# Optimization experiments

Measured on AMD Instinct MI355X. Metric: run time of the kernel, lower is better.

The kernel has to match this reference:

```python
import jax, jax.numpy as jnp
import numpy as np

N, L, S, H, D = 2, 2048, 2048, 8, 64

def elu_feature_map(x):
    return jax.nn.elu(x) + 1.0

def setup_inputs() -> dict:
    key = jax.random.key(0)
    k1, k2, k3, k4, k5 = jax.random.split(key, 5)
    return {
        "queries": jax.random.normal(k1, (N, L, H, D), dtype=jnp.float32),
        "keys": jax.random.normal(k2, (N, S, H, D), dtype=jnp.float32),
        "values": jax.random.normal(k3, (N, S, H, D), dtype=jnp.float32),
        "q_mask": jnp.ones((N, L), dtype=jnp.float32),
        "kv_mask": jnp.ones((N, S), dtype=jnp.float32),
        "W": jax.random.normal(k4, (1, 2), dtype=jnp.float32) * 0.5,  # nn.Linear(2,1) weight
        "b": jax.random.normal(k5, (1,), dtype=jnp.float32) * 0.5,    # nn.Linear(2,1) bias
    }

def reference(queries, keys, values, q_mask, kv_mask, W, b):
    # feature map: elu(x) + 1
    Q = elu_feature_map(queries) * q_mask[:, :, None, None]   # [N,L,H,D]
    K = elu_feature_map(keys) * kv_mask[:, :, None, None]     # [N,S,H,D]
    queries_m = queries * q_mask[:, :, None, None]
    values_m = values * kv_mask[:, :, None, None]  # masked but unused downstream (as in original)
    del values_m
    # full QK score tensor [N,L,S,H]
    qk = jnp.einsum('nlhd,nshd->nlsh', Q, K)
    qk_mean = jnp.mean(qk, axis=2)  # [N,L,H]
    qk_max = jnp.max(qk, axis=2)    # [N,L,H]
    stats = jnp.stack([qk_mean, qk_max], axis=-1)  # [N,L,H,2]
    gate = jax.nn.sigmoid(jnp.einsum('nlhe,oe->nlho', stats, W) + b)  # [N,L,H,1]
    atten = gate[..., 0]  # [N,L,H]
    return queries_m * atten[..., None]  # [N,L,H,D]
```

## Files before the change

### kernel.cpp

```cpp
#include <hip/hip_runtime.h>
#include <math.h>

#define N_ 2
#define L_ 2048
#define S_ 2048
#define H_ 8
#define D_ 64

#define BLK_L 256
#define BS 64
#define SSPLIT 4

typedef __attribute__((ext_vector_type(8))) short short8;
typedef _Float16 half8 __attribute__((ext_vector_type(8)));
typedef __attribute__((ext_vector_type(16))) float floatx16;

__device__ __forceinline__ float feat(float x) {
    return x > 0.0f ? x + 1.0f : __expf(x);
}
__device__ __forceinline__ void gload_lds16(const void* g, void* l) {
    __builtin_amdgcn_global_load_lds(
        (__attribute__((address_space(1))) void*)g,
        (__attribute__((address_space(3))) void*)l, 16, 0, 0);
}

__global__ __launch_bounds__(256) void featk_kernel(
        const float* __restrict__ K, const float* __restrict__ kvmask,
        short* __restrict__ Khi, short* __restrict__ Klo,
        float* __restrict__ Ksum) {
    __shared__ float sm[64][68];
    __shared__ float sm2[256];
    int nh = blockIdx.x;
    int z  = blockIdx.y;
    int n = nh >> 3, h = nh & 7;
    int t = threadIdx.x;
    int srow = t >> 2, g = t & 3;
    int s = z * 64 + srow;

    float km = kvmask[n * S_ + s];
    const float* kp = K + (((size_t)n * S_ + s) * H_ + h) * D_ + g * 16;
    float fv[16];
    #pragma unroll
    for (int j = 0; j < 4; ++j) {
        float4 v = *(const float4*)(kp + j * 4);
        fv[4 * j + 0] = feat(v.x) * km;
        fv[4 * j + 1] = feat(v.y) * km;
        fv[4 * j + 2] = feat(v.z) * km;
        fv[4 * j + 3] = feat(v.w) * km;
    }
    half8 h0, h1, l0, l1;
    #pragma unroll
    for (int j = 0; j < 8; ++j) {
        _Float16 hb = (_Float16)fv[j];
        h0[j] = hb;  l0[j] = (_Float16)(fv[j] - (float)hb);
        _Float16 hb2 = (_Float16)fv[8 + j];
        h1[j] = hb2; l1[j] = (_Float16)(fv[8 + j] - (float)hb2);
    }
    size_t rowbase = ((size_t)nh * S_ + s) * (size_t)D_;
    int rx = srow & 7;
    *(half8*)(Khi + rowbase + ((((2 * g)    ) ^ rx) << 3)) = h0;
    *(half8*)(Khi + rowbase + ((((2 * g) + 1) ^ rx) << 3)) = h1;
    *(half8*)(Klo + rowbase + ((((2 * g)    ) ^ rx) << 3)) = l0;
    *(half8*)(Klo + rowbase + ((((2 * g) + 1) ^ rx) << 3)) = l1;

    #pragma unroll
    for (int j2 = 0; j2 < 4; ++j2)
        *(float4*)&sm[srow][g * 16 + 4 * j2] =
            make_float4(fv[4 * j2], fv[4 * j2 + 1], fv[4 * j2 + 2], fv[4 * j2 + 3]);
    __syncthreads();
    {
        int d = t & 63, grp = t >> 6;
        float part = 0.f;
        #pragma unroll
        for (int k = 0; k < 16; ++k) part += sm[grp * 16 + k][d];
        sm2[t] = part;
    }
    __syncthreads();
    if (t < 64) {
        float tot = sm2[t] + sm2[t + 64] + sm2[t + 128] + sm2[t + 192];
        atomicAdd(&Ksum[nh * 64 + t], tot);
    }
}

__global__ __launch_bounds__(256, 2) void rowmax_mfma(
        const float* __restrict__ Q, const short* __restrict__ Khi,
        const short* __restrict__ Klo, const float* __restrict__ qmask,
        float* __restrict__ rowmaxg) {
    __shared__ __align__(16) char lds[2][16384];

    int flat = blockIdx.x + (blockIdx.y << 3) + (blockIdx.z << 7);
    int nid  = ((flat & 7) << 6) | (flat >> 3);
    int bx = nid & 7;
    int nh = (nid >> 3) & 15;
    int z  = nid >> 7;

    int n = nh >> 3, h = nh & 7;
    int t = threadIdx.x;
    int w = t >> 6, lane = t & 63;
    int c31 = lane & 31, hi32 = lane >> 5;
    int lblock = bx * BLK_L;

    const char* gKh = (const char*)Khi + ((size_t)nh * S_ + (size_t)z * (S_ / SSPLIT)) * 128;
    const char* gKl = (const char*)Klo + ((size_t)nh * S_ + (size_t)z * (S_ / SSPLIT)) * 128;
    int sidx = w << 2;

    auto stage = [&](int tile, int db) {
        #pragma unroll
        for (int c = 0; c < 4; ++c) {
            int idx = sidx | c;
            const char* src = (idx < 8 ? gKh : gKl)
                              + tile * 8192 + ((idx & 7) << 10) + (lane << 4);
            gload_lds16(src, &lds[db][idx << 10]);
        }
    };

    stage(0, 0);

    half8 Ah[2][4], Al[2][4];
    #pragma unroll
    for (int lt = 0; lt < 2; ++lt) {
        int lrow = lblock + w * 64 + lt * 32 + c31;
        float qm = qmask[n * L_ + lrow];
        const float* qp = Q + (((size_t)n * L_ + lrow) * H_ + h) * D_ + hi32 * 8;
        #pragma unroll
        for (int ks = 0; ks < 4; ++ks) {
            float4 v0 = *(const float4*)(qp + ks * 16);
            float4 v1 = *(const float4*)(qp + ks * 16 + 4);
            float fv[8];
            fv[0] = feat(v0.x) * qm; fv[1] = feat(v0.y) * qm;
            fv[2] = feat(v0.z) * qm; fv[3] = feat(v0.w) * qm;
            fv[4] = feat(v1.x) * qm; fv[5] = feat(v1.y) * qm;
            fv[6] = feat(v1.z) * qm; fv[7] = feat(v1.w) * qm;
            half8 hi, lo;
            #pragma unroll
            for (int j = 0; j < 8; ++j) {
                _Float16 hb = (_Float16)fv[j];
                hi[j] = hb;
                lo[j] = (_Float16)(fv[j] - (float)hb);
            }
            Ah[lt][ks] = hi;
            Al[lt][ks] = lo;
        }
    }

    int boff[2][4];
    #pragma unroll
    for (int st = 0; st < 2; ++st)
        #pragma unroll
        for (int ks = 0; ks < 4; ++ks) {
            int row = st * 32 + c31;
            boff[st][ks] = row * 128 + (((2 * ks + hi32) ^ (row & 7)) << 4);
        }

    float rmax[2][16];
    #pragma unroll
    for (int i = 0; i < 2; ++i)
        #pragma unroll
        for (int r = 0; r < 16; ++r) rmax[i][r] = 0.f;

    const floatx16 Z = {0.f};

    __syncthreads();

    const int tiles = S_ / SSPLIT / BS;
    for (int tile = 0; tile < tiles; ++tile) {
        int db = tile & 1;
        if (tile + 1 < tiles) stage(tile + 1, db ^ 1);
        const char* hp = lds[db];
        const char* lp = lds[db] + 8192;
        #pragma unroll
        for (int st = 0; st < 2; ++st) {
            half8 Bh[4], Bl[4];
            #pragma unroll
            for (int ks = 0; ks < 4; ++ks) {
                Bh[ks] = *(const half8*)(hp + boff[st][ks]);
                Bl[ks] = *(const half8*)(lp + boff[st][ks]);
            }
            #pragma unroll
            for (int lt = 0; lt < 2; ++lt) {
                floatx16 acc;
                acc = __builtin_amdgcn_mfma_f32_32x32x16_f16(Ah[lt][0], Bh[0], Z,   0, 0, 0);
                acc = __builtin_amdgcn_mfma_f32_32x32x16_f16(Ah[lt][1], Bh[1], acc, 0, 0, 0);
                acc = __builtin_amdgcn_mfma_f32_32x32x16_f16(Ah[lt][2], Bh[2], acc, 0, 0, 0);
                acc = __builtin_amdgcn_mfma_f32_32x32x16_f16(Ah[lt][3], Bh[3], acc, 0, 0, 0);
                acc = __builtin_amdgcn_mfma_f32_32x32x16_f16(Ah[lt][0], Bl[0], acc, 0, 0, 0);
                acc = __builtin_amdgcn_mfma_f32_32x32x16_f16(Ah[lt][1], Bl[1], acc, 0, 0, 0);
                acc = __builtin_amdgcn_mfma_f32_32x32x16_f16(Ah[lt][2], Bl[2], acc, 0, 0, 0);
                acc = __builtin_amdgcn_mfma_f32_32x32x16_f16(Ah[lt][3], Bl[3], acc, 0, 0, 0);
                acc = __builtin_amdgcn_mfma_f32_32x32x16_f16(Al[lt][0], Bh[0], acc, 0, 0, 0);
                acc = __builtin_amdgcn_mfma_f32_32x32x16_f16(Al[lt][1], Bh[1], acc, 0, 0, 0);
                acc = __builtin_amdgcn_mfma_f32_32x32x16_f16(Al[lt][2], Bh[2], acc, 0, 0, 0);
                acc = __builtin_amdgcn_mfma_f32_32x32x16_f16(Al[lt][3], Bh[3], acc, 0, 0, 0);
                #pragma unroll
                for (int r = 0; r < 16; ++r)
                    rmax[lt][r] = fmaxf(rmax[lt][r], acc[r]);
            }
        }
        __syncthreads();
    }

    #pragma unroll
    for (int lt = 0; lt < 2; ++lt)
        #pragma unroll
        for (int r = 0; r < 16; ++r) {
            float m = rmax[lt][r];
            m = fmaxf(m, __shfl_xor(m, 1, 64));
            m = fmaxf(m, __shfl_xor(m, 2, 64));
            m = fmaxf(m, __shfl_xor(m, 4, 64));
            m = fmaxf(m, __shfl_xor(m, 8, 64));
            m = fmaxf(m, __shfl_xor(m, 16, 64));
            if (c31 == 0) {
                int l = lblock + w * 64 + lt * 32 + (r & 3) + ((r >> 2) << 3) + (hi32 << 2);
                atomicMax((unsigned*)&rowmaxg[(size_t)nh * L_ + l],
                          __float_as_uint(m));
            }
        }
}

__global__ __launch_bounds__(256) void finalize_kernel(
        const float* __restrict__ Q, const float* __restrict__ qmask,
        const float* __restrict__ Ksum, const float* __restrict__ rowmaxg,
        const float* __restrict__ W, const float* __restrict__ b,
        float* __restrict__ out) {
    int t = threadIdx.x;
    int lane = t & 63;
    int wid = (blockIdx.x << 2) | (t >> 6);
    int n = wid / (L_ * H_);
    int lh = wid % (L_ * H_);
    int l = lh / H_, h = lh % H_;

    float q = Q[(size_t)wid * 64 + lane];
    float qm = qmask[n * L_ + l];
    float p = feat(q) * qm * Ksum[(n * H_ + h) * 64 + lane];
    #pragma unroll
    for (int off = 32; off > 0; off >>= 1)
        p += __shfl_xor(p, off, 64);
    float mean = p * (1.0f / S_);
    float mx = rowmaxg[((size_t)n * H_ + h) * L_ + l];
    float zz = W[0] * mean + W[1] * mx + b[0];
    float g = 1.0f / (1.0f + __expf(-zz));
    out[(size_t)wid * 64 + lane] = q * qm * g;
}

extern "C" void kernel_launch(void* const* d_in, const int* in_sizes, int n_in,
                              void* d_out, int out_size, void* d_ws, size_t ws_size,
                              hipStream_t stream) {
    const float* Q      = (const float*)d_in[0];
    const float* K      = (const float*)d_in[1];
    const float* qmask  = (const float*)d_in[3];
    const float* kvmask = (const float*)d_in[4];
    const float* W      = (const float*)d_in[5];
    const float* b      = (const float*)d_in[6];
    float* out = (float*)d_out;

    float* Ksum   = (float*)d_ws;
    float* rowmax = (float*)d_ws + 1024;
    short* Khi    = (short*)((float*)d_ws + 1024 + 32768);
    short* Klo    = Khi + (size_t)N_ * H_ * S_ * D_;

    hipMemsetAsync(d_ws, 0, (1024 + (size_t)N_ * H_ * L_) * sizeof(float), stream);

    featk_kernel<<<dim3(N_ * H_, S_ / 64), 256, 0, stream>>>(K, kvmask, Khi, Klo, Ksum);
    rowmax_mfma<<<dim3(L_ / BLK_L, N_ * H_, SSPLIT), 256, 0, stream>>>(
        Q, Khi, Klo, qmask, rowmax);
    finalize_kernel<<<dim3(N_ * L_ * H_ / 4), 256, 0, stream>>>(
        Q, qmask, Ksum, rowmax, W, b, out);
}
```

Baseline: 118.5 us.

## Drop memset and atomics, use bf16 split MFMA, 512-thread blocks, vectorized finalize

Removes the workspace memset by writing per-block partial K sums and per-split row maxima instead of atomics, and reduces them later: Ksum inside the rowmax kernel, the four split maxima in finalize. Switches the hi/lo split product from fp16 to bf16 MFMA with manual round-to-nearest conversion. Doubles the rowmax block to 512 threads with one 32-row tile per wave, and vectorizes finalize to float4 per thread with 16-lane reductions. The bf16 hi/lo split keeps fewer mantissa bits than fp16 hi/lo, which risks accuracy. The Ksum reduction inside rowmax_mfma is not ordered before finalize within the same kernel, but finalize runs as a later launch, so it is safe.

```diff
diff --git a/kernel.cpp b/kernel.cpp
--- a/kernel.cpp
+++ b/kernel.cpp
@@ -12,11 +12,18 @@
 #define SSPLIT 4
 
 typedef __attribute__((ext_vector_type(8))) short short8;
-typedef _Float16 half8 __attribute__((ext_vector_type(8)));
 typedef __attribute__((ext_vector_type(16))) float floatx16;
 
 __device__ __forceinline__ float feat(float x) {
     return x > 0.0f ? x + 1.0f : __expf(x);
+}
+__device__ __forceinline__ short f2bf(float x) {
+    unsigned u = __float_as_uint(x);
+    unsigned r = (u + 0x7fffu + ((u >> 16) & 1u)) >> 16;
+    return (short)r;
+}
+__device__ __forceinline__ float bf2f(short h) {
+    return __uint_as_float(((unsigned)(unsigned short)h) << 16);
 }
 __device__ __forceinline__ void gload_lds16(const void* g, void* l) {
     __builtin_amdgcn_global_load_lds(
@@ -27,7 +34,7 @@
 __global__ __launch_bounds__(256) void featk_kernel(
         const float* __restrict__ K, const float* __restrict__ kvmask,
         short* __restrict__ Khi, short* __restrict__ Klo,
-        float* __restrict__ Ksum) {
+        float* __restrict__ Kpart) {
     __shared__ float sm[64][68];
     __shared__ float sm2[256];
     int nh = blockIdx.x;
@@ -48,20 +55,20 @@
         fv[4 * j + 2] = feat(v.z) * km;
         fv[4 * j + 3] = feat(v.w) * km;
     }
-    half8 h0, h1, l0, l1;
+    short8 h0, h1, l0, l1;
     #pragma unroll
     for (int j = 0; j < 8; ++j) {
-        _Float16 hb = (_Float16)fv[j];
-        h0[j] = hb;  l0[j] = (_Float16)(fv[j] - (float)hb);
-        _Float16 hb2 = (_Float16)fv[8 + j];
-        h1[j] = hb2; l1[j] = (_Float16)(fv[8 + j] - (float)hb2);
+        short hb = f2bf(fv[j]);
+        h0[j] = hb;  l0[j] = f2bf(fv[j] - bf2f(hb));
+        short hb2 = f2bf(fv[8 + j]);
+        h1[j] = hb2; l1[j] = f2bf(fv[8 + j] - bf2f(hb2));
     }
     size_t rowbase = ((size_t)nh * S_ + s) * (size_t)D_;
     int rx = srow & 7;
-    *(half8*)(Khi + rowbase + ((((2 * g)    ) ^ rx) << 3)) = h0;
-    *(half8*)(Khi + rowbase + ((((2 * g) + 1) ^ rx) << 3)) = h1;
-    *(half8*)(Klo + rowbase + ((((2 * g)    ) ^ rx) << 3)) = l0;
-    *(half8*)(Klo + rowbase + ((((2 * g) + 1) ^ rx) << 3)) = l1;
+    *(short8*)(Khi + rowbase + ((((2 * g)    ) ^ rx) << 3)) = h0;
+    *(short8*)(Khi + rowbase + ((((2 * g) + 1) ^ rx) << 3)) = h1;
+    *(short8*)(Klo + rowbase + ((((2 * g)    ) ^ rx) << 3)) = l0;
+    *(short8*)(Klo + rowbase + ((((2 * g) + 1) ^ rx) << 3)) = l1;
 
     #pragma unroll
     for (int j2 = 0; j2 < 4; ++j2)
@@ -78,14 +85,15 @@
     __syncthreads();
     if (t < 64) {
         float tot = sm2[t] + sm2[t + 64] + sm2[t + 128] + sm2[t + 192];
-        atomicAdd(&Ksum[nh * 64 + t], tot);
-    }
-}
-
-__global__ __launch_bounds__(256, 2) void rowmax_mfma(
+        Kpart[(nh * 32 + z) * 64 + t] = tot;
+    }
+}
+
+__global__ __launch_bounds__(512) void rowmax_mfma(
         const float* __restrict__ Q, const short* __restrict__ Khi,
         const short* __restrict__ Klo, const float* __restrict__ qmask,
-        float* __restrict__ rowmaxg) {
+        const float* __restrict__ Kpart, float* __restrict__ Ksum,
+        float* __restrict__ rmax_part) {
     __shared__ __align__(16) char lds[2][16384];
 
     int flat = blockIdx.x + (blockIdx.y << 3) + (blockIdx.z << 7);
@@ -100,13 +108,21 @@
     int c31 = lane & 31, hi32 = lane >> 5;
     int lblock = bx * BLK_L;
 
+    if (bx == 0 && z == 0 && t < 64) {
+        float s = 0.f;
+        #pragma unroll
+        for (int zz = 0; zz < 32; ++zz)
+            s += Kpart[(nh * 32 + zz) * 64 + t];
+        Ksum[nh * 64 + t] = s;
+    }
+
     const char* gKh = (const char*)Khi + ((size_t)nh * S_ + (size_t)z * (S_ / SSPLIT)) * 128;
     const char* gKl = (const char*)Klo + ((size_t)nh * S_ + (size_t)z * (S_ / SSPLIT)) * 128;
-    int sidx = w << 2;
+    int sidx = w << 1;
 
     auto stage = [&](int tile, int db) {
         #pragma unroll
-        for (int c = 0; c < 4; ++c) {
+        for (int c = 0; c < 2; ++c) {
             int idx = sidx | c;
             const char* src = (idx < 8 ? gKh : gKl)
                               + tile * 8192 + ((idx & 7) << 10) + (lane << 4);
@@ -116,10 +132,9 @@
 
     stage(0, 0);
 
-    half8 Ah[2][4], Al[2][4];
-    #pragma unroll
-    for (int lt = 0; lt < 2; ++lt) {
-        int lrow = lblock + w * 64 + lt * 32 + c31;
+    short8 Ah[4], Al[4];
+    {
+        int lrow = lblock + w * 32 + c31;
         float qm = qmask[n * L_ + lrow];
         const float* qp = Q + (((size_t)n * L_ + lrow) * H_ + h) * D_ + hi32 * 8;
         #pragma unroll
@@ -131,15 +146,15 @@
             fv[2] = feat(v0.z) * qm; fv[3] = feat(v0.w) * qm;
             fv[4] = feat(v1.x) * qm; fv[5] = feat(v1.y) * qm;
             fv[6] = feat(v1.z) * qm; fv[7] = feat(v1.w) * qm;
-            half8 hi, lo;
+            short8 hi, lo;
             #pragma unroll
             for (int j = 0; j < 8; ++j) {
-                _Float16 hb = (_Float16)fv[j];
+                short hb = f2bf(fv[j]);
                 hi[j] = hb;
-                lo[j] = (_Float16)(fv[j] - (float)hb);
+                lo[j] = f2bf(fv[j] - bf2f(hb));
             }
-            Ah[lt][ks] = hi;
-            Al[lt][ks] = lo;
+            Ah[ks] = hi;
+            Al[ks] = lo;
         }
     }
 
@@ -152,11 +167,9 @@
             boff[st][ks] = row * 128 + (((2 * ks + hi32) ^ (row & 7)) << 4);
         }
 
-    float rmax[2][16];
-    #pragma unroll
-    for (int i = 0; i < 2; ++i)
-        #pragma unroll
-        for (int r = 0; r < 16; ++r) rmax[i][r] = 0.f;
+    float rmax[16];
+    #pragma unroll
+    for (int r = 0; r < 16; ++r) rmax[r] = 0.f;
 
     const floatx16 Z = {0.f};
 
@@ -170,76 +183,83 @@
         const char* lp = lds[db] + 8192;
         #pragma unroll
         for (int st = 0; st < 2; ++st) {
-            half8 Bh[4], Bl[4];
+            short8 Bh[4], Bl[4];
             #pragma unroll
             for (int ks = 0; ks < 4; ++ks) {
-                Bh[ks] = *(const half8*)(hp + boff[st][ks]);
-                Bl[ks] = *(const half8*)(lp + boff[st][ks]);
+                Bh[ks] = *(const short8*)(hp + boff[st][ks]);
+                Bl[ks] = *(const short8*)(lp + boff[st][ks]);
             }
+            floatx16 acc;
+            acc = __builtin_amdgcn_mfma_f32_32x32x16_bf16(Ah[0], Bh[0], Z,   0, 0, 0);
+            acc = __builtin_amdgcn_mfma_f32_32x32x16_bf16(Ah[1], Bh[1], acc, 0, 0, 0);
+            acc = __builtin_amdgcn_mfma_f32_32x32x16_bf16(Ah[2], Bh[2], acc, 0, 0, 0);
+            acc = __builtin_amdgcn_mfma_f32_32x32x16_bf16(Ah[3], Bh[3], acc, 0, 0, 0);
+            acc = __builtin_amdgcn_mfma_f32_32x32x16_bf16(Ah[0], Bl[0], acc, 0, 0, 0);
+            acc = __builtin_amdgcn_mfma_f32_32x32x16_bf16(Ah[1], Bl[1], acc, 0, 0, 0);
+            acc = __builtin_amdgcn_mfma_f32_32x32x16_bf16(Ah[2], Bl[2], acc, 0, 0, 0);
+            acc = __builtin_amdgcn_mfma_f32_32x32x16_bf16(Ah[3], Bl[3], acc, 0, 0, 0);
+            acc = __builtin_amdgcn_mfma_f32_32x32x16_bf16(Al[0], Bh[0], acc, 0, 0, 0);
+            acc = __builtin_amdgcn_mfma_f32_32x32x16_bf16(Al[1], Bh[1], acc, 0, 0, 0);
+            acc = __builtin_amdgcn_mfma_f32_32x32x16_bf16(Al[2], Bh[2], acc, 0, 0, 0);
+            acc = __builtin_amdgcn_mfma_f32_32x32x16_bf16(Al[3], Bh[3], acc, 0, 0, 0);
             #pragma unroll
-            for (int lt = 0; lt < 2; ++lt) {
-                floatx16 acc;
-                acc = __builtin_amdgcn_mfma_f32_32x32x16_f16(Ah[lt][0], Bh[0], Z,   0, 0, 0);
-                acc = __builtin_amdgcn_mfma_f32_32x32x16_f16(Ah[lt][1], Bh[1], acc, 0, 0, 0);
-                acc = __builtin_amdgcn_mfma_f32_32x32x16_f16(Ah[lt][2], Bh[2], acc, 0, 0, 0);
-                acc = __builtin_amdgcn_mfma_f32_32x32x16_f16(Ah[lt][3], Bh[3], acc, 0, 0, 0);
-                acc = __builtin_amdgcn_mfma_f32_32x32x16_f16(Ah[lt][0], Bl[0], acc, 0, 0, 0);
-                acc = __builtin_amdgcn_mfma_f32_32x32x16_f16(Ah[lt][1], Bl[1], acc, 0, 0, 0);
-                acc = __builtin_amdgcn_mfma_f32_32x32x16_f16(Ah[lt][2], Bl[2], acc, 0, 0, 0);
-                acc = __builtin_amdgcn_mfma_f32_32x32x16_f16(Ah[lt][3], Bl[3], acc, 0, 0, 0);
-                acc = __builtin_amdgcn_mfma_f32_32x32x16_f16(Al[lt][0], Bh[0], acc, 0, 0, 0);
-                acc = __builtin_amdgcn_mfma_f32_32x32x16_f16(Al[lt][1], Bh[1], acc, 0, 0, 0);
-                acc = __builtin_amdgcn_mfma_f32_32x32x16_f16(Al[lt][2], Bh[2], acc, 0, 0, 0);
-                acc = __builtin_amdgcn_mfma_f32_32x32x16_f16(Al[lt][3], Bh[3], acc, 0, 0, 0);
-                #pragma unroll
-                for (int r = 0; r < 16; ++r)
-                    rmax[lt][r] = fmaxf(rmax[lt][r], acc[r]);
-            }
+            for (int r = 0; r < 16; ++r)
+                rmax[r] = fmaxf(rmax[r], acc[r]);
         }
         __syncthreads();
     }
 
     #pragma unroll
-    for (int lt = 0; lt < 2; ++lt)
-        #pragma unroll
-        for (int r = 0; r < 16; ++r) {
-            float m = rmax[lt][r];
-            m = fmaxf(m, __shfl_xor(m, 1, 64));
-            m = fmaxf(m, __shfl_xor(m, 2, 64));
-            m = fmaxf(m, __shfl_xor(m, 4, 64));
-            m = fmaxf(m, __shfl_xor(m, 8, 64));
-            m = fmaxf(m, __shfl_xor(m, 16, 64));
-            if (c31 == 0) {
-                int l = lblock + w * 64 + lt * 32 + (r & 3) + ((r >> 2) << 3) + (hi32 << 2);
-                atomicMax((unsigned*)&rowmaxg[(size_t)nh * L_ + l],
-                          __float_as_uint(m));
-            }
-        }
+    for (int r = 0; r < 16; ++r) {
+        float m = rmax[r];
+        m = fmaxf(m, __shfl_xor(m, 1, 64));
+        m = fmaxf(m, __shfl_xor(m, 2, 64));
+        m = fmaxf(m, __shfl_xor(m, 4, 64));
+        m = fmaxf(m, __shfl_xor(m, 8, 64));
+        m = fmaxf(m, __shfl_xor(m, 16, 64));
+        if (c31 == 0) {
+            int l = lblock + w * 32 + (r & 3) + ((r >> 2) << 3) + (hi32 << 2);
+            rmax_part[((size_t)(z * 16 + nh)) * L_ + l] = m;
+        }
+    }
 }
 
 __global__ __launch_bounds__(256) void finalize_kernel(
         const float* __restrict__ Q, const float* __restrict__ qmask,
-        const float* __restrict__ Ksum, const float* __restrict__ rowmaxg,
+        const float* __restrict__ Ksum, const float* __restrict__ rmax_part,
         const float* __restrict__ W, const float* __restrict__ b,
         float* __restrict__ out) {
     int t = threadIdx.x;
-    int lane = t & 63;
-    int wid = (blockIdx.x << 2) | (t >> 6);
+    int fid = blockIdx.x * 256 + t;
+    int wid = fid >> 4;
+    int sub = fid & 15;
     int n = wid / (L_ * H_);
     int lh = wid % (L_ * H_);
     int l = lh / H_, h = lh % H_;
-
-    float q = Q[(size_t)wid * 64 + lane];
+    int nh = n * H_ + h;
+
+    float4 q4 = ((const float4*)Q)[fid];
     float qm = qmask[n * L_ + l];
-    float p = feat(q) * qm * Ksum[(n * H_ + h) * 64 + lane];
-    #pragma unroll
-    for (int off = 32; off > 0; off >>= 1)
-        p += __shfl_xor(p, off, 64);
+    float4 ks4 = ((const float4*)(Ksum + nh * 64))[sub];
+    float p = feat(q4.x) * ks4.x + feat(q4.y) * ks4.y
+            + feat(q4.z) * ks4.z + feat(q4.w) * ks4.w;
+    p *= qm;
+    p += __shfl_xor(p, 1, 64);
+    p += __shfl_xor(p, 2, 64);
+    p += __shfl_xor(p, 4, 64);
+    p += __shfl_xor(p, 8, 64);
     float mean = p * (1.0f / S_);
-    float mx = rowmaxg[((size_t)n * H_ + h) * L_ + l];
+    float mx = fmaxf(
+        fmaxf(rmax_part[((size_t)(0 * 16 + nh)) * L_ + l],
+              rmax_part[((size_t)(1 * 16 + nh)) * L_ + l]),
+        fmaxf(rmax_part[((size_t)(2 * 16 + nh)) * L_ + l],
+              rmax_part[((size_t)(3 * 16 + nh)) * L_ + l]));
     float zz = W[0] * mean + W[1] * mx + b[0];
     float g = 1.0f / (1.0f + __expf(-zz));
-    out[(size_t)wid * 64 + lane] = q * qm * g;
+    float4 o;
+    o.x = q4.x * qm * g; o.y = q4.y * qm * g;
+    o.z = q4.z * qm * g; o.w = q4.w * qm * g;
+    ((float4*)out)[fid] = o;
 }
 
 extern "C" void kernel_launch(void* const* d_in, const int* in_sizes, int n_in,
@@ -253,16 +273,15 @@
     const float* b      = (const float*)d_in[6];
     float* out = (float*)d_out;
 
-    float* Ksum   = (float*)d_ws;
-    float* rowmax = (float*)d_ws + 1024;
-    short* Khi    = (short*)((float*)d_ws + 1024 + 32768);
-    short* Klo    = Khi + (size_t)N_ * H_ * S_ * D_;
-
-    hipMemsetAsync(d_ws, 0, (1024 + (size_t)N_ * H_ * L_) * sizeof(float), stream);
-
-    featk_kernel<<<dim3(N_ * H_, S_ / 64), 256, 0, stream>>>(K, kvmask, Khi, Klo, Ksum);
-    rowmax_mfma<<<dim3(L_ / BLK_L, N_ * H_, SSPLIT), 256, 0, stream>>>(
-        Q, Khi, Klo, qmask, rowmax);
-    finalize_kernel<<<dim3(N_ * L_ * H_ / 4), 256, 0, stream>>>(
-        Q, qmask, Ksum, rowmax, W, b, out);
-}
+    float* Ksum      = (float*)d_ws;
+    float* Kpart     = Ksum + 1024;
+    float* rmax_part = Kpart + 32768;
+    short* Khi       = (short*)(rmax_part + 131072);
+    short* Klo       = Khi + (size_t)N_ * H_ * S_ * D_;
+
+    featk_kernel<<<dim3(N_ * H_, S_ / 64), 256, 0, stream>>>(K, kvmask, Khi, Klo, Kpart);
+    rowmax_mfma<<<dim3(L_ / BLK_L, N_ * H_, SSPLIT), 512, 0, stream>>>(
+        Q, Khi, Klo, qmask, Kpart, Ksum, rmax_part);
+    finalize_kernel<<<dim3((N_ * L_ * H_ * D_ / 4) / 256), 256, 0, stream>>>(
+        Q, qmask, Ksum, rmax_part, W, b, out);
+}
```

Result: slower. 162.4 us (+37.1%).
